# Kernel tuning notes

Hardware: AMD Instinct MI355X
Metric: run time of the kernel (lower is better)

Reference implementation:

```python
import jax, jax.numpy as jnp
import numpy as np

B, H, W = 2, 1024, 1024
NNZ = 100000          # active pixels
C = 16                # max electron count bins (dense dim of sparse logits)
CIN, CH = 128, 128    # in_pixel_features, beta_distn_hidden_dim
THR = 0.95            # count_cdf_threshold
QMAX = NNZ * (C - 1)  # static upper bound on ragged query count


def setup_inputs() -> dict:
    key = jax.random.key(0)
    ks = jax.random.split(key, 4)
    rng = np.random.default_rng(0)
    per = NNZ // B
    idx_list = []
    for b in range(B):
        flat = np.sort(rng.choice(H * W, per, replace=False))  # unique active sites
        idx_list.append(np.stack([np.full(per, b), flat // W, flat % W]))
    occ_indices = jnp.asarray(np.concatenate(idx_list, 1), jnp.int32)  # [3, NNZ]
    occ_values = jax.random.normal(ks[0], (NNZ, C), jnp.float32) * 2.0
    pixel_values = jax.random.normal(ks[1], (NNZ, CIN), jnp.float32)
    w1 = jax.random.normal(ks[2], (3, 3, CIN, CH), jnp.float32) / np.sqrt(9 * CIN)
    b1 = jnp.zeros((CH,), jnp.float32)
    w2 = jax.random.normal(ks[3], (CH, 4), jnp.float32) / np.sqrt(CH)
    b2 = jnp.zeros((4,), jnp.float32)
    return dict(occ_values=occ_values, occ_indices=occ_indices,
                pixel_values=pixel_values, w1=w1, b1=b1, w2=w2, b2=b2)


def reference(occ_values, occ_indices, pixel_values, w1, b1, w2, b2):
    # --- cdf_threshold_min_predicted_electrons ---
    probs = jax.nn.softmax(occ_values, -1)                      # sparse softmax over dense count dim
    cdf = jnp.cumsum(probs, -1)
    over = cdf > THR
    temp = jnp.arange(C, 0, -1) * over
    counts = jnp.argmax(temp, 1)                                # [NNZ] min count over cdf threshold

    # --- repeat_interleave(indices, counts) -> padded ragged queries ---
    cum = jnp.cumsum(counts)
    total = cum[-1]
    q = jnp.arange(QMAX)
    valid = q < total
    src = jnp.minimum(jnp.searchsorted(cum, q, side='right'), NNZ - 1)  # [QMAX]
    query_indices = occ_indices[:, src].T                       # [QMAX, 3] (b, i, j)

    # --- dense hash grid: (b,i,j) -> active-site row ---
    b_, i_, j_ = occ_indices
    flat = (b_ * H + i_) * W + j_
    grid = jnp.full((B * H * W,), -1, jnp.int32).at[flat].set(
        jnp.arange(NNZ, dtype=jnp.int32))

    # --- SubMConv2d(CIN->CH, k=3): output at active sites only ---
    acc = jnp.zeros((NNZ, CH), pixel_values.dtype) + b1
    for di in (-1, 0, 1):
        for dj in (-1, 0, 1):
            ni, nj = i_ + di, j_ + dj
            inb = (ni >= 0) & (ni < H) & (nj >= 0) & (nj < W)
            nflat = (b_ * H + jnp.clip(ni, 0, H - 1)) * W + jnp.clip(nj, 0, W - 1)
            nidx = jnp.where(inb, grid[nflat], -1)
            m = nidx >= 0
            feat = jnp.where(m[:, None], pixel_values[jnp.maximum(nidx, 0)], 0.0)
            acc = acc + feat @ w1[di + 1, dj + 1]
    h = jax.nn.relu(acc)
    logp = h @ w2 + b2                                          # [NNZ, 4] SubMConv2d(CH->4, k=1)

    # --- gather_from_sparse_tensor at query pixels ---
    qflat = (query_indices[:, 0] * H + query_indices[:, 1]) * W + query_indices[:, 2]
    row = jnp.maximum(grid[qflat], 0)
    params = jnp.exp(logp[row])                                 # [QMAX, 4]
    xa, xb, ya, yb = jnp.split(params, 4, -1)

    # --- Beta rsample (reparameterized gamma-based sampler) ---
    k1, k2 = jax.random.split(jax.random.key(42))
    x = jax.random.beta(k1, xa, xb)
    y = jax.random.beta(k2, ya, yb)
    off = jnp.concatenate([x, y], -1) * valid[:, None]          # [QMAX, 2]
    query_indices = jnp.where(valid[:, None], query_indices, 0)
    return query_indices, off
```

## Files before the change

kernel.cpp:

```cpp
#include <hip/hip_runtime.h>
#include <cstdint>

#define NNZ   100000
#define CBINS 16
#define HD    1024
#define WD    1024
#define CIN   128
#define CH    128
#define QMAX  (NNZ * (CBINS - 1))

struct Key { uint32_t a, b; };

__device__ __forceinline__ uint32_t rotl32(uint32_t v, int r) {
  return (v << r) | (v >> (32 - r));
}

__device__ __forceinline__ void tf_block(uint32_t k0, uint32_t k1,
                                         uint32_t x0, uint32_t x1,
                                         uint32_t& o0, uint32_t& o1) {
  uint32_t ks2 = k0 ^ k1 ^ 0x1BD11BDAu;
  x0 += k0; x1 += k1;
#define TF_RND(r) { x0 += x1; x1 = rotl32(x1, r); x1 ^= x0; }
  TF_RND(13) TF_RND(15) TF_RND(26) TF_RND(6)
  x0 += k1;  x1 += ks2 + 1u;
  TF_RND(17) TF_RND(29) TF_RND(16) TF_RND(24)
  x0 += ks2; x1 += k0 + 2u;
  TF_RND(13) TF_RND(15) TF_RND(26) TF_RND(6)
  x0 += k0;  x1 += k1 + 3u;
  TF_RND(17) TF_RND(29) TF_RND(16) TF_RND(24)
  x0 += k1;  x1 += ks2 + 4u;
  TF_RND(13) TF_RND(15) TF_RND(26) TF_RND(6)
  x0 += ks2; x1 += k0 + 5u;
#undef TF_RND
  o0 = x0; o1 = x1;
}

__device__ __forceinline__ Key tf_key(Key k, uint32_t chi, uint32_t clo) {
  Key r; tf_block(k.a, k.b, chi, clo, r.a, r.b); return r;
}

__device__ __forceinline__ uint32_t random_bits32(Key k) {
  uint32_t a, b; tf_block(k.a, k.b, 0u, 0u, a, b); return a ^ b;
}

__device__ __forceinline__ float bits_to_u01(uint32_t bits) {
  uint32_t fb = (bits >> 9) | 0x3F800000u;
  return __uint_as_float(fb) - 1.0f;
}

__device__ float erfinv32(float x) {
#pragma clang fp contract(off)
  float w = -log1pf(-(x * x));
  float p;
  if (w < 5.0f) {
    w = w - 2.5f;
    p = 2.81022636e-08f;
    p = 3.43273939e-07f  + p * w;
    p = -3.5233877e-06f  + p * w;
    p = -4.39150654e-06f + p * w;
    p = 0.00021858087f   + p * w;
    p = -0.00125372503f  + p * w;
    p = -0.00417768164f  + p * w;
    p = 0.246640727f     + p * w;
    p = 1.50140941f      + p * w;
  } else {
    w = sqrtf(w) - 3.0f;
    p = -0.000200214257f;
    p = 0.000100950558f  + p * w;
    p = 0.00134934322f   + p * w;
    p = -0.00367342844f  + p * w;
    p = 0.00573950773f   + p * w;
    p = -0.0076224613f   + p * w;
    p = 0.00943887047f   + p * w;
    p = 1.00167406f      + p * w;
    p = 2.83297682f      + p * w;
  }
  return p * x;
}

__device__ __forceinline__ float uniform01(Key k) {
  return bits_to_u01(random_bits32(k));
}

__device__ __forceinline__ float normal_f32(Key k) {
#pragma clang fp contract(off)
  const float LO = -0x1.fffffep-1f;
  float f = bits_to_u01(random_bits32(k));
  float u = f * 2.0f + LO;
  u = fmaxf(LO, u);
  return 1.4142135623730951f * erfinv32(u);
}

__device__ float loggamma_one(Key key, float alpha_orig) {
#pragma clang fp contract(off)
  bool boost = (alpha_orig >= 1.0f);
  float alpha = boost ? alpha_orig : (alpha_orig + 1.0f);
  const float OT = 0.3333333333333333f;
  float d = alpha - OT;
  float c = OT / sqrtf(d);

  Key knext = tf_key(key, 0u, 0u);
  Key ksub  = tf_key(key, 0u, 1u);
  float u_boost = uniform01(ksub);

  float X = 0.0f, V = 1.0f, U = 2.0f;
  while (true) {
    bool c1 = U >= (1.0f - 0.0331f * (X * X));
    bool c2 = logf(U) >= (X * 0.5f + d * ((1.0f - V) + logf(V)));
    if (!(c1 && c2)) break;
    Key kcur = knext;
    knext    = tf_key(kcur, 0u, 0u);
    Key xk   = tf_key(kcur, 0u, 1u);
    Key Uk   = tf_key(kcur, 0u, 2u);
    float x = 0.0f, v = -1.0f;
    while (v <= 0.0f) {
      Key nxk = tf_key(xk, 0u, 0u);
      Key sk  = tf_key(xk, 0u, 1u);
      xk = nxk;
      x = normal_f32(sk);
      v = 1.0f + x * c;
    }
    X = x * x;
    V = (v * v) * v;
    U = uniform01(Uk);
  }
  float log_samples = logf(d) + logf(V);
  float log_boost = 0.0f;
  if (!boost && u_boost != 0.0f)
    log_boost = logf(u_boost) * (1.0f / alpha_orig);
  return log_samples + log_boost;
}

__device__ float beta_sample(Key ka, Key kb, uint32_t q, float a, float b) {
#pragma clang fp contract(off)
  Key ga = tf_key(ka, 0u, q);
  Key gb = tf_key(kb, 0u, q);
  float la = loggamma_one(ga, a);
  float lb = loggamma_one(gb, b);
  float lm = fmaxf(la, lb);
  float ea = expf(la - lm);
  float eb = expf(lb - lm);
  return ea / (ea + eb);
}


__device__ __forceinline__ void ascan16(const float* a, float* out) {
  float r[8], r2[4], r3[2];
#pragma unroll
  for (int i = 0; i < 8; ++i) r[i] = a[2 * i] + a[2 * i + 1];
#pragma unroll
  for (int i = 0; i < 4; ++i) r2[i] = r[2 * i] + r[2 * i + 1];
  r3[0] = r2[0] + r2[1];
  r3[1] = r2[2] + r2[3];
  float r4 = r3[0] + r3[1];
  float s3[2] = {r3[0], r4};
  float s2[4] = {r2[0], s3[0], s3[0] + r2[2], s3[1]};
  float sr[8] = {r[0],          s2[0],
                 s2[0] + r[2],  s2[1],
                 s2[1] + r[4],  s2[2],
                 s2[2] + r[6],  s2[3]};
  out[0] = a[0];
#pragma unroll
  for (int i = 0; i < 8; ++i) out[2 * i + 1] = sr[i];
#pragma unroll
  for (int i = 0; i < 7; ++i) out[2 * i + 2] = sr[i] + a[2 * i + 2];
}

__global__ __launch_bounds__(256)
void counts_kernel(const float* __restrict__ occ_values,
                   const int* __restrict__ occ_idx,
                   int* __restrict__ counts,
                   int* __restrict__ flatall) {
  int i = blockIdx.x * 256 + threadIdx.x;
  if (i >= NNZ) return;
  const float4* vp = (const float4*)(occ_values + (size_t)i * CBINS);
  float4 q0 = vp[0], q1 = vp[1], q2 = vp[2], q3 = vp[3];
  float v[16] = {q0.x,q0.y,q0.z,q0.w, q1.x,q1.y,q1.z,q1.w,
                 q2.x,q2.y,q2.z,q2.w, q3.x,q3.y,q3.z,q3.w};
  float m = v[0];
#pragma unroll
  for (int k = 1; k < 16; ++k) m = fmaxf(m, v[k]);
  float e[16];
#pragma unroll
  for (int k = 0; k < 16; ++k) e[k] = expf(v[k] - m);
  float s = 0.0f;
#pragma unroll
  for (int k = 0; k < 16; ++k) s += e[k];
  float p[16], cdf[16];
#pragma unroll
  for (int k = 0; k < 16; ++k) p[k] = e[k] / s;
  ascan16(p, cdf);
  int cnt = 0; bool found = false;
#pragma unroll
  for (int k = 0; k < 16; ++k) {
    if (!found && cdf[k] > 0.95f) { found = true; cnt = k; }
  }
  counts[i] = found ? cnt : 0;
  int b_ = occ_idx[i], i_ = occ_idx[NNZ + i], j_ = occ_idx[2 * NNZ + i];
  flatall[i] = (b_ * HD + i_) * WD + j_;
}

#define SCAN_B 1024
__global__ __launch_bounds__(SCAN_B)
void scan_block_kernel(const int* __restrict__ counts, int* __restrict__ cum,
                       int* __restrict__ bsums) {
  __shared__ int sh[SCAN_B];
  int t = threadIdx.x;
  int i = blockIdx.x * SCAN_B + t;
  sh[t] = (i < NNZ) ? counts[i] : 0;
  __syncthreads();
  for (int off = 1; off < SCAN_B; off <<= 1) {
    int add = (t >= off) ? sh[t - off] : 0;
    __syncthreads();
    sh[t] += add;
    __syncthreads();
  }
  if (i < NNZ) cum[i] = sh[t];
  if (t == SCAN_B - 1) bsums[blockIdx.x] = sh[t];
}

__global__ void scan_sums_kernel(int* bsums, int nblocks) {
  __shared__ int sh[128];
  int t = threadIdx.x;
  sh[t] = (t < nblocks) ? bsums[t] : 0;
  __syncthreads();
  for (int off = 1; off < 128; off <<= 1) {
    int add = (t >= off) ? sh[t - off] : 0;
    __syncthreads();
    sh[t] += add;
    __syncthreads();
  }
  if (t < nblocks) bsums[t] = sh[t];
}

__global__ __launch_bounds__(SCAN_B)
void scan_add_kernel(int* cum, const int* __restrict__ bsums) {
  int b = blockIdx.x;
  if (b == 0) return;
  int i = b * SCAN_B + threadIdx.x;
  if (i < NNZ) cum[i] += bsums[b - 1];
}

__device__ __forceinline__ int find_site(const int* __restrict__ flatall, int tval) {
  int lo = 0, hi = NNZ;
  while (lo < hi) {
    int mid = (lo + hi) >> 1;
    if (flatall[mid] < tval) lo = mid + 1; else hi = mid;
  }
  return (lo < NNZ && flatall[lo] == tval) ? lo : -1;
}

__global__ __launch_bounds__(256)
void neighbors_kernel(const int* __restrict__ occ_idx,
                      const int* __restrict__ flatall,
                      int* __restrict__ rlist,
                      int* __restrict__ asl,
                      int* __restrict__ nact) {
  int s = blockIdx.x * 256 + threadIdx.x;
  if (s >= NNZ) return;
  int b_ = occ_idx[s], i_ = occ_idx[NNZ + s], j_ = occ_idx[2 * NNZ + s];
  int m = 0;
  bool any = false;
#pragma unroll
  for (int di = -1; di <= 1; ++di) {
#pragma unroll
    for (int dj = -1; dj <= 1; ++dj) {
      if (di == 0 && dj == 0) continue;
      int ni = i_ + di, nj = j_ + dj, r = -1;
      if ((unsigned)ni < HD && (unsigned)nj < WD)
        r = find_site(flatall, (b_ * HD + ni) * WD + nj);
      rlist[(size_t)s * 8 + m] = r;
      any |= (r >= 0);
      ++m;
    }
  }
  if (any) {
    int slot = atomicAdd(nact, 1);
    asl[slot] = s;
  }
}

__global__ __launch_bounds__(256)
void scatter_src_kernel(const int* __restrict__ counts,
                        const int* __restrict__ cum,
                        int* __restrict__ srcmap) {
  int s = blockIdx.x * 256 + threadIdx.x;
  if (s >= NNZ) return;
  int e = cum[s], c = counts[s];
  for (int q = e - c; q < e; ++q) srcmap[q] = s;
}

#define TSITES 64
__global__ __launch_bounds__(256)
void conv_center_kernel(const float* __restrict__ pv,
                        const float* __restrict__ w1,
                        const float* __restrict__ b1,
                        float* __restrict__ h) {
  __shared__ float Wsh[32 * CH];
  int base = blockIdx.x * TSITES;
  int t = threadIdx.x;
  int ts = t >> 5, to = t & 31;

  float acc[8][4];
  {
    float4 bv = *(const float4*)(b1 + to * 4);
#pragma unroll
    for (int s8 = 0; s8 < 8; ++s8) {
      acc[s8][0] = bv.x; acc[s8][1] = bv.y; acc[s8][2] = bv.z; acc[s8][3] = bv.w;
    }
  }

  const float* prow[8];
#pragma unroll
  for (int s8 = 0; s8 < 8; ++s8) {
    int site = base + s8 * 8 + ts;
    if (site > NNZ - 1) site = NNZ - 1;
    prow[s8] = pv + (size_t)site * CIN;
  }

  const float* wc = w1 + 4 * CIN * CH;
  for (int k0 = 0; k0 < CIN; k0 += 32) {
    __syncthreads();
    {
      const float4* srcw = (const float4*)(wc + (size_t)k0 * CH);
      float4* dstw = (float4*)Wsh;
#pragma unroll
      for (int rep = 0; rep < 4; ++rep) dstw[t + rep * 256] = srcw[t + rep * 256];
    }
    __syncthreads();
#pragma unroll
    for (int kk = 0; kk < 32; kk += 4) {
      float4 wq0 = ((const float4*)(Wsh + (kk + 0) * CH))[to];
      float4 wq1 = ((const float4*)(Wsh + (kk + 1) * CH))[to];
      float4 wq2 = ((const float4*)(Wsh + (kk + 2) * CH))[to];
      float4 wq3 = ((const float4*)(Wsh + (kk + 3) * CH))[to];
#pragma unroll
      for (int s8 = 0; s8 < 8; ++s8) {
        float4 a4 = *(const float4*)(prow[s8] + k0 + kk);
        acc[s8][0] += a4.x * wq0.x; acc[s8][1] += a4.x * wq0.y;
        acc[s8][2] += a4.x * wq0.z; acc[s8][3] += a4.x * wq0.w;
        acc[s8][0] += a4.y * wq1.x; acc[s8][1] += a4.y * wq1.y;
        acc[s8][2] += a4.y * wq1.z; acc[s8][3] += a4.y * wq1.w;
        acc[s8][0] += a4.z * wq2.x; acc[s8][1] += a4.z * wq2.y;
        acc[s8][2] += a4.z * wq2.z; acc[s8][3] += a4.z * wq2.w;
        acc[s8][0] += a4.w * wq3.x; acc[s8][1] += a4.w * wq3.y;
        acc[s8][2] += a4.w * wq3.z; acc[s8][3] += a4.w * wq3.w;
      }
    }
  }

#pragma unroll
  for (int s8 = 0; s8 < 8; ++s8) {
    int site = base + s8 * 8 + ts;
    if (site < NNZ)
      *(float4*)(h + (size_t)site * CH + 4 * to) =
          make_float4(acc[s8][0], acc[s8][1], acc[s8][2], acc[s8][3]);
  }
}

__global__ __launch_bounds__(256)
void conv_corr_kernel(const float* __restrict__ pv,
                      const float* __restrict__ w1,
                      const int* __restrict__ rlist,
                      const int* __restrict__ asl,
                      const int* __restrict__ nact,
                      float* __restrict__ h) {
  int t = threadIdx.x;
  int l = t & 63;
  int wave = (blockIdx.x << 2) + (t >> 6);
  int nwaves = gridDim.x << 2;
  int n = *nact;
  for (int e = wave; e < n; e += nwaves) {
    int s = asl[e];
    float* hr = h + (size_t)s * CH;
    float2 hv = *(const float2*)(hr + 2 * l);
    float ha = hv.x, hb = hv.y;
#pragma unroll
    for (int m = 0; m < 8; ++m) {
      int r = rlist[(size_t)s * 8 + m];
      if (r < 0) continue;
      int tap = (m < 4) ? m : m + 1;
      const float* wt = w1 + (size_t)tap * CIN * CH + 2 * l;
      const float* pr = pv + (size_t)r * CIN;
#pragma unroll 8
      for (int k = 0; k < CIN; k += 4) {
        float4 pq = *(const float4*)(pr + k);
        float2 wv0 = *(const float2*)(wt + (k + 0) * CH);
        float2 wv1 = *(const float2*)(wt + (k + 1) * CH);
        float2 wv2 = *(const float2*)(wt + (k + 2) * CH);
        float2 wv3 = *(const float2*)(wt + (k + 3) * CH);
        ha += pq.x * wv0.x; hb += pq.x * wv0.y;
        ha += pq.y * wv1.x; hb += pq.y * wv1.y;
        ha += pq.z * wv2.x; hb += pq.z * wv2.y;
        ha += pq.w * wv3.x; hb += pq.w * wv3.y;
      }
    }
    *(float2*)(hr + 2 * l) = make_float2(ha, hb);
  }
}

#define HP 132
__global__ __launch_bounds__(256)
void head_kernel(const float* __restrict__ h,
                 const float* __restrict__ w2,
                 const float* __restrict__ b2,
                 float* __restrict__ logp) {
  __shared__ float hs[TSITES * HP];
  int base = blockIdx.x * TSITES;
  int t = threadIdx.x;
#pragma unroll
  for (int rep = 0; rep < 8; ++rep) {
    int idx = t + rep * 256;
    int s = idx >> 5, c = idx & 31;
    int site = base + s;
    if (site > NNZ - 1) site = NNZ - 1;
    float4 v = *(const float4*)(h + (size_t)site * CH + 4 * c);
    *(float4*)(hs + s * HP + 4 * c) = v;
  }
  __syncthreads();
  int s = t & 63, j = t >> 6;
  int site = base + s;
  if (site < NNZ) {
    const float* hr = hs + s * HP;
    float sum = 0.0f;
    for (int o = 0; o < CH; o += 2) {
      float2 hv = *(const float2*)(hr + o);
      sum += fmaxf(hv.x, 0.f) * w2[(o + 0) * 4 + j];
      sum += fmaxf(hv.y, 0.f) * w2[(o + 1) * 4 + j];
    }
    logp[(size_t)site * 4 + j] = sum + b2[j];
  }
}

__global__ __launch_bounds__(256)
void query_kernel(const int* __restrict__ occ_idx,
                  const int* __restrict__ cum,
                  const int* __restrict__ srcmap,
                  const float* __restrict__ logp,
                  float* __restrict__ out_idx,
                  float* __restrict__ out_off) {
  int q = blockIdx.x * 256 + threadIdx.x;
  if (q >= QMAX) return;
  int total = cum[NNZ - 1];
  if (q >= total) {
    out_idx[(size_t)q * 3 + 0] = 0.0f;
    out_idx[(size_t)q * 3 + 1] = 0.0f;
    out_idx[(size_t)q * 3 + 2] = 0.0f;
    out_off[(size_t)q * 2 + 0] = 0.0f;
    out_off[(size_t)q * 2 + 1] = 0.0f;
    return;
  }
  int src = srcmap[q];
  out_idx[(size_t)q * 3 + 0] = (float)occ_idx[src];
  out_idx[(size_t)q * 3 + 1] = (float)occ_idx[NNZ + src];
  out_idx[(size_t)q * 3 + 2] = (float)occ_idx[2 * NNZ + src];

  float4 lp = *(const float4*)(logp + (size_t)src * 4);
  float p0 = expf(lp.x), p1 = expf(lp.y), p2 = expf(lp.z), p3 = expf(lp.w);

  Key root{0u, 42u};
  Key k1  = tf_key(root, 0u, 0u);
  Key k2  = tf_key(root, 0u, 1u);
  Key kxa = tf_key(k1, 0u, 0u);
  Key kxb = tf_key(k1, 0u, 1u);
  Key kya = tf_key(k2, 0u, 0u);
  Key kyb = tf_key(k2, 0u, 1u);

  float x = beta_sample(kxa, kxb, (uint32_t)q, p0, p1);
  float y = beta_sample(kya, kyb, (uint32_t)q, p2, p3);
  out_off[(size_t)q * 2 + 0] = x;
  out_off[(size_t)q * 2 + 1] = y;
}

extern "C" void kernel_launch(void* const* d_in, const int* in_sizes, int n_in,
                              void* d_out, int out_size, void* d_ws, size_t ws_size,
                              hipStream_t stream) {
  const float* occ_values = (const float*)d_in[0];
  const int*   occ_idx    = (const int*)d_in[1];
  const float* pv         = (const float*)d_in[2];
  const float* w1         = (const float*)d_in[3];
  const float* b1         = (const float*)d_in[4];
  const float* w2         = (const float*)d_in[5];
  const float* b2         = (const float*)d_in[6];

  char* ws = (char*)d_ws;
  auto alignup = [](size_t x) { return (x + 255) & ~(size_t)255; };
  size_t o = 0;
  int* counts  = (int*)(ws + o); o += alignup((size_t)NNZ * 4);
  int* cum     = (int*)(ws + o); o += alignup((size_t)NNZ * 4);
  int* flatall = (int*)(ws + o); o += alignup((size_t)NNZ * 4);
  int* bsums   = (int*)(ws + o); o += alignup(128 * 4);
  float* logp  = (float*)(ws + o); o += alignup((size_t)NNZ * 4 * sizeof(float));
  int* rlist   = (int*)(ws + o); o += alignup((size_t)NNZ * 8 * 4);
  int* srcmap  = (int*)(ws + o); o += alignup((size_t)QMAX * 4);
  int* asl     = (int*)(ws + o); o += alignup((size_t)NNZ * 4);
  int* nact    = (int*)(ws + o); o += alignup(256);
  float* h     = (float*)(ws + o); o += alignup((size_t)NNZ * CH * sizeof(float));

  float* out_idx = (float*)d_out;
  float* out_off = out_idx + (size_t)QMAX * 3;

  counts_kernel<<<(NNZ + 255) / 256, 256, 0, stream>>>(occ_values, occ_idx,
                                                       counts, flatall);
  int nsb = (NNZ + SCAN_B - 1) / SCAN_B;
  scan_block_kernel<<<nsb, SCAN_B, 0, stream>>>(counts, cum, bsums);
  scan_sums_kernel<<<1, 128, 0, stream>>>(bsums, nsb);
  scan_add_kernel<<<nsb, SCAN_B, 0, stream>>>(cum, bsums);
  hipMemsetAsync(nact, 0, 4, stream);
  neighbors_kernel<<<(NNZ + 255) / 256, 256, 0, stream>>>(occ_idx, flatall,
                                                          rlist, asl, nact);
  scatter_src_kernel<<<(NNZ + 255) / 256, 256, 0, stream>>>(counts, cum, srcmap);
  conv_center_kernel<<<(NNZ + TSITES - 1) / TSITES, 256, 0, stream>>>(
      pv, w1, b1, h);
  conv_corr_kernel<<<2048, 256, 0, stream>>>(pv, w1, rlist, asl, nact, h);
  head_kernel<<<(NNZ + TSITES - 1) / TSITES, 256, 0, stream>>>(h, w2, b2, logp);
  query_kernel<<<(QMAX + 255) / 256, 256, 0, stream>>>(occ_idx, cum, srcmap,
                                                       logp, out_idx, out_off);
}
```

Measured before the change: 689.4 us.

## Group neighbor-conv work into per-tap pair lists with LDS-resident weights

Instead of one wave per active site that reads all eight neighbor-tap weight matrices from global memory, neighbors are binned by tap into capped pair lists. A new pair kernel stages one tap's 128x128 weight matrix in shared memory and computes each neighbor's feature-times-weight product into a pair buffer. The head kernel then sums those partial products into each site's hidden row before applying the output head. This is meant to improve weight reuse and load balance, at the cost of an extra pair buffer written and read, plus atomic contention on eight counters. Pairs beyond the fixed 8192-per-tap cap are silently dropped, so correctness depends on input sparsity staying low.

```diff
diff --git a/kernel.cpp b/kernel.cpp
--- a/kernel.cpp
+++ b/kernel.cpp
@@ -8,6 +8,7 @@
 #define CIN   128
 #define CH    128
 #define QMAX  (NNZ * (CBINS - 1))
+#define PCAP  8192
 
 struct Key { uint32_t a, b; };
 
@@ -253,14 +254,13 @@
 __global__ __launch_bounds__(256)
 void neighbors_kernel(const int* __restrict__ occ_idx,
                       const int* __restrict__ flatall,
-                      int* __restrict__ rlist,
-                      int* __restrict__ asl,
-                      int* __restrict__ nact) {
+                      int* __restrict__ pl_r,
+                      int* __restrict__ ncnt,
+                      int* __restrict__ pairidx) {
   int s = blockIdx.x * 256 + threadIdx.x;
   if (s >= NNZ) return;
   int b_ = occ_idx[s], i_ = occ_idx[NNZ + s], j_ = occ_idx[2 * NNZ + s];
   int m = 0;
-  bool any = false;
 #pragma unroll
   for (int di = -1; di <= 1; ++di) {
 #pragma unroll
@@ -269,14 +269,17 @@
       int ni = i_ + di, nj = j_ + dj, r = -1;
       if ((unsigned)ni < HD && (unsigned)nj < WD)
         r = find_site(flatall, (b_ * HD + ni) * WD + nj);
-      rlist[(size_t)s * 8 + m] = r;
-      any |= (r >= 0);
+      int idx = -1;
+      if (r >= 0) {
+        int slot = atomicAdd(&ncnt[m], 1);
+        if (slot < PCAP) {
+          pl_r[m * PCAP + slot] = r;
+          idx = m * PCAP + slot;
+        }
+      }
+      pairidx[(size_t)s * 8 + m] = idx;
       ++m;
     }
-  }
-  if (any) {
-    int slot = atomicAdd(nact, 1);
-    asl[slot] = s;
   }
 }
 
@@ -359,49 +362,49 @@
 }
 
 __global__ __launch_bounds__(256)
-void conv_corr_kernel(const float* __restrict__ pv,
-                      const float* __restrict__ w1,
-                      const int* __restrict__ rlist,
-                      const int* __restrict__ asl,
-                      const int* __restrict__ nact,
-                      float* __restrict__ h) {
-  int t = threadIdx.x;
-  int l = t & 63;
-  int wave = (blockIdx.x << 2) + (t >> 6);
-  int nwaves = gridDim.x << 2;
-  int n = *nact;
-  for (int e = wave; e < n; e += nwaves) {
-    int s = asl[e];
-    float* hr = h + (size_t)s * CH;
-    float2 hv = *(const float2*)(hr + 2 * l);
-    float ha = hv.x, hb = hv.y;
-#pragma unroll
-    for (int m = 0; m < 8; ++m) {
-      int r = rlist[(size_t)s * 8 + m];
-      if (r < 0) continue;
-      int tap = (m < 4) ? m : m + 1;
-      const float* wt = w1 + (size_t)tap * CIN * CH + 2 * l;
-      const float* pr = pv + (size_t)r * CIN;
-#pragma unroll 8
-      for (int k = 0; k < CIN; k += 4) {
-        float4 pq = *(const float4*)(pr + k);
-        float2 wv0 = *(const float2*)(wt + (k + 0) * CH);
-        float2 wv1 = *(const float2*)(wt + (k + 1) * CH);
-        float2 wv2 = *(const float2*)(wt + (k + 2) * CH);
-        float2 wv3 = *(const float2*)(wt + (k + 3) * CH);
-        ha += pq.x * wv0.x; hb += pq.x * wv0.y;
-        ha += pq.y * wv1.x; hb += pq.y * wv1.y;
-        ha += pq.z * wv2.x; hb += pq.z * wv2.y;
-        ha += pq.w * wv3.x; hb += pq.w * wv3.y;
-      }
-    }
-    *(float2*)(hr + 2 * l) = make_float2(ha, hb);
+void pair_kernel(const float* __restrict__ pv,
+                 const float* __restrict__ w1,
+                 const int* __restrict__ pl_r,
+                 const int* __restrict__ ncnt,
+                 float* __restrict__ pairout) {
+  __shared__ float Wsh[CIN * CH];
+  int tm = blockIdx.x & 7;
+  int tap = (tm < 4) ? tm : tm + 1;
+  {
+    const float4* src = (const float4*)(w1 + (size_t)tap * CIN * CH);
+    float4* dst = (float4*)Wsh;
+    for (int i = threadIdx.x; i < CIN * CH / 4; i += 256) dst[i] = src[i];
+  }
+  __syncthreads();
+  int n = ncnt[tm];
+  if (n > PCAP) n = PCAP;
+  int w = threadIdx.x >> 6, l = threadIdx.x & 63;
+  int nb = gridDim.x >> 3;
+  for (int e = (blockIdx.x >> 3) * 4 + w; e < n; e += nb * 4) {
+    int r = pl_r[tm * PCAP + e];
+    const float* pr = pv + (size_t)r * CIN;
+    float a0 = 0.0f, a1 = 0.0f;
+    for (int k = 0; k < CIN; k += 4) {
+      float4 pq = *(const float4*)(pr + k);
+      float2 w0 = *(const float2*)(Wsh + (k + 0) * CH + 2 * l);
+      float2 w1v = *(const float2*)(Wsh + (k + 1) * CH + 2 * l);
+      float2 w2v = *(const float2*)(Wsh + (k + 2) * CH + 2 * l);
+      float2 w3v = *(const float2*)(Wsh + (k + 3) * CH + 2 * l);
+      a0 += pq.x * w0.x;  a1 += pq.x * w0.y;
+      a0 += pq.y * w1v.x; a1 += pq.y * w1v.y;
+      a0 += pq.z * w2v.x; a1 += pq.z * w2v.y;
+      a0 += pq.w * w3v.x; a1 += pq.w * w3v.y;
+    }
+    *(float2*)(pairout + (size_t)(tm * PCAP + e) * CH + 2 * l) =
+        make_float2(a0, a1);
   }
 }
 
 #define HP 132
 __global__ __launch_bounds__(256)
 void head_kernel(const float* __restrict__ h,
+                 const int* __restrict__ pairidx,
+                 const float* __restrict__ pairout,
                  const float* __restrict__ w2,
                  const float* __restrict__ b2,
                  float* __restrict__ logp) {
@@ -416,6 +419,26 @@
     if (site > NNZ - 1) site = NNZ - 1;
     float4 v = *(const float4*)(h + (size_t)site * CH + 4 * c);
     *(float4*)(hs + s * HP + 4 * c) = v;
+  }
+  __syncthreads();
+  {
+    int s = t >> 2, g = t & 3;
+    int site = base + s;
+    if (site < NNZ) {
+      float* hr = hs + s * HP + g * 32;
+#pragma unroll
+      for (int m = 0; m < 8; ++m) {
+        int idx = pairidx[(size_t)site * 8 + m];
+        if (idx < 0) continue;
+        const float* po = pairout + (size_t)idx * CH + g * 32;
+#pragma unroll
+        for (int c = 0; c < 32; c += 4) {
+          float4 v = *(const float4*)(po + c);
+          hr[c + 0] += v.x; hr[c + 1] += v.y;
+          hr[c + 2] += v.z; hr[c + 3] += v.w;
+        }
+      }
+    }
   }
   __syncthreads();
   int s = t & 63, j = t >> 6;
@@ -486,16 +509,17 @@
   char* ws = (char*)d_ws;
   auto alignup = [](size_t x) { return (x + 255) & ~(size_t)255; };
   size_t o = 0;
-  int* counts  = (int*)(ws + o); o += alignup((size_t)NNZ * 4);
-  int* cum     = (int*)(ws + o); o += alignup((size_t)NNZ * 4);
-  int* flatall = (int*)(ws + o); o += alignup((size_t)NNZ * 4);
-  int* bsums   = (int*)(ws + o); o += alignup(128 * 4);
-  float* logp  = (float*)(ws + o); o += alignup((size_t)NNZ * 4 * sizeof(float));
-  int* rlist   = (int*)(ws + o); o += alignup((size_t)NNZ * 8 * 4);
-  int* srcmap  = (int*)(ws + o); o += alignup((size_t)QMAX * 4);
-  int* asl     = (int*)(ws + o); o += alignup((size_t)NNZ * 4);
-  int* nact    = (int*)(ws + o); o += alignup(256);
-  float* h     = (float*)(ws + o); o += alignup((size_t)NNZ * CH * sizeof(float));
+  int* counts   = (int*)(ws + o); o += alignup((size_t)NNZ * 4);
+  int* cum      = (int*)(ws + o); o += alignup((size_t)NNZ * 4);
+  int* flatall  = (int*)(ws + o); o += alignup((size_t)NNZ * 4);
+  int* bsums    = (int*)(ws + o); o += alignup(128 * 4);
+  float* logp   = (float*)(ws + o); o += alignup((size_t)NNZ * 4 * sizeof(float));
+  int* pairidx  = (int*)(ws + o); o += alignup((size_t)NNZ * 8 * 4);
+  int* srcmap   = (int*)(ws + o); o += alignup((size_t)QMAX * 4);
+  int* pl_r     = (int*)(ws + o); o += alignup((size_t)8 * PCAP * 4);
+  int* ncnt     = (int*)(ws + o); o += alignup(256);
+  float* h      = (float*)(ws + o); o += alignup((size_t)NNZ * CH * sizeof(float));
+  float* pairout= (float*)(ws + o); o += alignup((size_t)8 * PCAP * CH * sizeof(float));
 
   float* out_idx = (float*)d_out;
   float* out_off = out_idx + (size_t)QMAX * 3;
@@ -506,14 +530,15 @@
   scan_block_kernel<<<nsb, SCAN_B, 0, stream>>>(counts, cum, bsums);
   scan_sums_kernel<<<1, 128, 0, stream>>>(bsums, nsb);
   scan_add_kernel<<<nsb, SCAN_B, 0, stream>>>(cum, bsums);
-  hipMemsetAsync(nact, 0, 4, stream);
+  hipMemsetAsync(ncnt, 0, 32, stream);
   neighbors_kernel<<<(NNZ + 255) / 256, 256, 0, stream>>>(occ_idx, flatall,
-                                                          rlist, asl, nact);
+                                                          pl_r, ncnt, pairidx);
   scatter_src_kernel<<<(NNZ + 255) / 256, 256, 0, stream>>>(counts, cum, srcmap);
   conv_center_kernel<<<(NNZ + TSITES - 1) / TSITES, 256, 0, stream>>>(
       pv, w1, b1, h);
-  conv_corr_kernel<<<2048, 256, 0, stream>>>(pv, w1, rlist, asl, nact, h);
-  head_kernel<<<(NNZ + TSITES - 1) / TSITES, 256, 0, stream>>>(h, w2, b2, logp);
+  pair_kernel<<<1024, 256, 0, stream>>>(pv, w1, pl_r, ncnt, pairout);
+  head_kernel<<<(NNZ + TSITES - 1) / TSITES, 256, 0, stream>>>(
+      h, pairidx, pairout, w2, b2, logp);
   query_kernel<<<(QMAX + 255) / 256, 256, 0, stream>>>(occ_idx, cum, srcmap,
                                                        logp, out_idx, out_off);
 }
```

Result: slower. 747.8 us (+8.5%).

## Compact gamma rejection-sampling retries into a shared-memory work queue

Applied to the files above, without the earlier changes.

Splits the Marsaglia-Tsang gamma sampler into a first attempt and a retry step. Rejected samples from all four gamma draws per query go into a block-level shared-memory queue, which all threads then drain cooperatively, so warps are no longer held up by a few lanes that keep looping. It also turns the fixed root-key derivations into compile-time constants so they are not recomputed per thread. The cost is extra shared memory, atomics and block barriers per retry round.

```diff
diff --git a/kernel.cpp b/kernel.cpp
--- a/kernel.cpp
+++ b/kernel.cpp
@@ -42,6 +42,31 @@
 __device__ __forceinline__ uint32_t random_bits32(Key k) {
   uint32_t a, b; tf_block(k.a, k.b, 0u, 0u, a, b); return a ^ b;
 }
+
+constexpr uint32_t rotlc(uint32_t v, int r) { return (v << r) | (v >> (32 - r)); }
+constexpr Key tf_key_c(Key k, uint32_t c0, uint32_t c1) {
+  uint32_t k0 = k.a, k1 = k.b, ks2 = k0 ^ k1 ^ 0x1BD11BDAu;
+  uint32_t x0 = c0 + k0, x1 = c1 + k1;
+  const int r1[4] = {13, 15, 26, 6}, r2[4] = {17, 29, 16, 24};
+  for (int i = 0; i < 4; ++i) { x0 += x1; x1 = rotlc(x1, r1[i]); x1 ^= x0; }
+  x0 += k1;  x1 += ks2 + 1u;
+  for (int i = 0; i < 4; ++i) { x0 += x1; x1 = rotlc(x1, r2[i]); x1 ^= x0; }
+  x0 += ks2; x1 += k0 + 2u;
+  for (int i = 0; i < 4; ++i) { x0 += x1; x1 = rotlc(x1, r1[i]); x1 ^= x0; }
+  x0 += k0;  x1 += k1 + 3u;
+  for (int i = 0; i < 4; ++i) { x0 += x1; x1 = rotlc(x1, r2[i]); x1 ^= x0; }
+  x0 += k1;  x1 += ks2 + 4u;
+  for (int i = 0; i < 4; ++i) { x0 += x1; x1 = rotlc(x1, r1[i]); x1 ^= x0; }
+  x0 += ks2; x1 += k0 + 5u;
+  return Key{x0, x1};
+}
+constexpr Key ROOTK{0u, 42u};
+constexpr Key K1C  = tf_key_c(ROOTK, 0u, 0u);
+constexpr Key K2C  = tf_key_c(ROOTK, 0u, 1u);
+constexpr Key KXA  = tf_key_c(K1C, 0u, 0u);
+constexpr Key KXB  = tf_key_c(K1C, 0u, 1u);
+constexpr Key KYA  = tf_key_c(K2C, 0u, 0u);
+constexpr Key KYB  = tf_key_c(K2C, 0u, 1u);
 
 __device__ __forceinline__ float bits_to_u01(uint32_t bits) {
   uint32_t fb = (bits >> 9) | 0x3F800000u;
@@ -91,56 +116,49 @@
   return 1.4142135623730951f * erfinv32(u);
 }
 
-__device__ float loggamma_one(Key key, float alpha_orig) {
+struct GState { Key knext; float d, c, boost; };
+
+__device__ bool gamma_iter(GState& st, float& result) {
+#pragma clang fp contract(off)
+  Key kcur = st.knext;
+  st.knext = tf_key(kcur, 0u, 0u);
+  Key xk   = tf_key(kcur, 0u, 1u);
+  Key Uk   = tf_key(kcur, 0u, 2u);
+  float x = 0.0f, v = -1.0f;
+  while (v <= 0.0f) {
+    Key nxk = tf_key(xk, 0u, 0u);
+    Key sk  = tf_key(xk, 0u, 1u);
+    xk = nxk;
+    x = normal_f32(sk);
+    v = 1.0f + x * st.c;
+  }
+  float X = x * x;
+  float V = (v * v) * v;
+  float U = uniform01(Uk);
+  bool c1 = U >= (1.0f - 0.0331f * (X * X));
+  bool c2 = logf(U) >= (X * 0.5f + st.d * ((1.0f - V) + logf(V)));
+  if (!(c1 && c2)) {
+    result = (logf(st.d) + logf(V)) + st.boost;
+    return true;
+  }
+  return false;
+}
+
+__device__ bool gamma_first(Key gkey, float alpha_orig, float& result,
+                            GState& st) {
 #pragma clang fp contract(off)
   bool boost = (alpha_orig >= 1.0f);
   float alpha = boost ? alpha_orig : (alpha_orig + 1.0f);
   const float OT = 0.3333333333333333f;
-  float d = alpha - OT;
-  float c = OT / sqrtf(d);
-
-  Key knext = tf_key(key, 0u, 0u);
-  Key ksub  = tf_key(key, 0u, 1u);
+  st.d = alpha - OT;
+  st.c = OT / sqrtf(st.d);
+  st.knext = tf_key(gkey, 0u, 0u);
+  Key ksub = tf_key(gkey, 0u, 1u);
   float u_boost = uniform01(ksub);
-
-  float X = 0.0f, V = 1.0f, U = 2.0f;
-  while (true) {
-    bool c1 = U >= (1.0f - 0.0331f * (X * X));
-    bool c2 = logf(U) >= (X * 0.5f + d * ((1.0f - V) + logf(V)));
-    if (!(c1 && c2)) break;
-    Key kcur = knext;
-    knext    = tf_key(kcur, 0u, 0u);
-    Key xk   = tf_key(kcur, 0u, 1u);
-    Key Uk   = tf_key(kcur, 0u, 2u);
-    float x = 0.0f, v = -1.0f;
-    while (v <= 0.0f) {
-      Key nxk = tf_key(xk, 0u, 0u);
-      Key sk  = tf_key(xk, 0u, 1u);
-      xk = nxk;
-      x = normal_f32(sk);
-      v = 1.0f + x * c;
-    }
-    X = x * x;
-    V = (v * v) * v;
-    U = uniform01(Uk);
-  }
-  float log_samples = logf(d) + logf(V);
-  float log_boost = 0.0f;
+  st.boost = 0.0f;
   if (!boost && u_boost != 0.0f)
-    log_boost = logf(u_boost) * (1.0f / alpha_orig);
-  return log_samples + log_boost;
-}
-
-__device__ float beta_sample(Key ka, Key kb, uint32_t q, float a, float b) {
-#pragma clang fp contract(off)
-  Key ga = tf_key(ka, 0u, q);
-  Key gb = tf_key(kb, 0u, q);
-  float la = loggamma_one(ga, a);
-  float lb = loggamma_one(gb, b);
-  float lm = fmaxf(la, lb);
-  float ea = expf(la - lm);
-  float eb = expf(lb - lm);
-  return ea / (ea + eb);
+    st.boost = logf(u_boost) * (1.0f / alpha_orig);
+  return gamma_iter(st, result);
 }
 
 
@@ -432,6 +450,8 @@
   }
 }
 
+struct QEntry { uint32_t ka, kb; float d, c, boost; int dest; };
+
 __global__ __launch_bounds__(256)
 void query_kernel(const int* __restrict__ occ_idx,
                   const int* __restrict__ cum,
@@ -439,37 +459,87 @@
                   const float* __restrict__ logp,
                   float* __restrict__ out_idx,
                   float* __restrict__ out_off) {
-  int q = blockIdx.x * 256 + threadIdx.x;
-  if (q >= QMAX) return;
+  __shared__ QEntry queue[1024];
+  __shared__ float res[1024];
+  __shared__ int qn;
+  int t = threadIdx.x;
+  if (t == 0) qn = 0;
+  int q = blockIdx.x * 256 + t;
+  bool inrange = q < QMAX;
   int total = cum[NNZ - 1];
-  if (q >= total) {
+  bool active = inrange && (q < total);
+
+  float alpha[4] = {1.0f, 1.0f, 1.0f, 1.0f};
+  if (active) {
+    int src = srcmap[q];
+    out_idx[(size_t)q * 3 + 0] = (float)occ_idx[src];
+    out_idx[(size_t)q * 3 + 1] = (float)occ_idx[NNZ + src];
+    out_idx[(size_t)q * 3 + 2] = (float)occ_idx[2 * NNZ + src];
+    float4 lp = *(const float4*)(logp + (size_t)src * 4);
+    alpha[0] = expf(lp.x); alpha[1] = expf(lp.y);
+    alpha[2] = expf(lp.z); alpha[3] = expf(lp.w);
+  } else if (inrange) {
     out_idx[(size_t)q * 3 + 0] = 0.0f;
     out_idx[(size_t)q * 3 + 1] = 0.0f;
     out_idx[(size_t)q * 3 + 2] = 0.0f;
     out_off[(size_t)q * 2 + 0] = 0.0f;
     out_off[(size_t)q * 2 + 1] = 0.0f;
-    return;
-  }
-  int src = srcmap[q];
-  out_idx[(size_t)q * 3 + 0] = (float)occ_idx[src];
-  out_idx[(size_t)q * 3 + 1] = (float)occ_idx[NNZ + src];
-  out_idx[(size_t)q * 3 + 2] = (float)occ_idx[2 * NNZ + src];
-
-  float4 lp = *(const float4*)(logp + (size_t)src * 4);
-  float p0 = expf(lp.x), p1 = expf(lp.y), p2 = expf(lp.z), p3 = expf(lp.w);
-
-  Key root{0u, 42u};
-  Key k1  = tf_key(root, 0u, 0u);
-  Key k2  = tf_key(root, 0u, 1u);
-  Key kxa = tf_key(k1, 0u, 0u);
-  Key kxb = tf_key(k1, 0u, 1u);
-  Key kya = tf_key(k2, 0u, 0u);
-  Key kyb = tf_key(k2, 0u, 1u);
-
-  float x = beta_sample(kxa, kxb, (uint32_t)q, p0, p1);
-  float y = beta_sample(kya, kyb, (uint32_t)q, p2, p3);
-  out_off[(size_t)q * 2 + 0] = x;
-  out_off[(size_t)q * 2 + 1] = y;
+  }
+  __syncthreads();
+
+  if (active) {
+    const Key gkeys[4] = {KXA, KXB, KYA, KYB};
+#pragma unroll
+    for (int g = 0; g < 4; ++g) {
+      Key gk = tf_key(gkeys[g], 0u, (uint32_t)q);
+      float r; GState st;
+      if (gamma_first(gk, alpha[g], r, st)) {
+        res[t * 4 + g] = r;
+      } else {
+        int slot = atomicAdd(&qn, 1);
+        queue[slot] = QEntry{st.knext.a, st.knext.b, st.d, st.c, st.boost,
+                             t * 4 + g};
+      }
+    }
+  }
+  __syncthreads();
+
+  int n = qn;
+  while (n > 0) {
+    QEntry my[4]; int myn = 0;
+    for (int i = t; i < n; i += 256) my[myn++] = queue[i];
+    __syncthreads();
+    if (t == 0) qn = 0;
+    __syncthreads();
+    for (int j = 0; j < myn; ++j) {
+      GState st; st.knext = Key{my[j].ka, my[j].kb};
+      st.d = my[j].d; st.c = my[j].c; st.boost = my[j].boost;
+      float r;
+      if (gamma_iter(st, r)) {
+        res[my[j].dest] = r;
+      } else {
+        int slot = atomicAdd(&qn, 1);
+        queue[slot] = QEntry{st.knext.a, st.knext.b, st.d, st.c, st.boost,
+                             my[j].dest};
+      }
+    }
+    __syncthreads();
+    n = qn;
+  }
+
+  if (active) {
+#pragma clang fp contract(off)
+    float la = res[t * 4 + 0], lb = res[t * 4 + 1];
+    float lm = fmaxf(la, lb);
+    float ea = expf(la - lm), eb = expf(lb - lm);
+    float x = ea / (ea + eb);
+    float lc = res[t * 4 + 2], ld = res[t * 4 + 3];
+    float lm2 = fmaxf(lc, ld);
+    float ec = expf(lc - lm2), ed = expf(ld - lm2);
+    float y = ec / (ec + ed);
+    out_off[(size_t)q * 2 + 0] = x;
+    out_off[(size_t)q * 2 + 1] = y;
+  }
 }
 
 extern "C" void kernel_launch(void* const* d_in, const int* in_sizes, int n_in,
```

After: 628.1 us. 8.9% less time.
